# Performance work log

Hardware: AMD Instinct MI355X
Metric: run time of the kernel (lower is better)

## Reference

```python
import jax, jax.numpy as jnp
import numpy as np

K = 10
EPS = 1e-5
SLOPE = 0.01
B, FIN, FOUT, N = 16, 128, 128, 2048


def _bn(x, g, b, axes):
    # training-mode batchnorm over given axes (channel dim is axis 1)
    m = jnp.mean(x, axis=axes, keepdims=True)
    v = jnp.var(x, axis=axes, keepdims=True)
    sh = [1] * x.ndim
    sh[1] = -1
    return (x - m) * jax.lax.rsqrt(v + EPS) * g.reshape(sh) + b.reshape(sh)


def _lrelu(x):
    return jnp.where(x >= 0, x, SLOPE * x)


def _conv1x1(x, W, b):
    return jnp.einsum('bcnk,oc->bonk', x, W) + b[None, :, None, None]


def _forward(x, pc, Wf, bf, gf, betaf, Wx, bx, gx, betax, Wa1, ba1, ga1, beta_a1, Wa2, ba2, ga2, beta_a2, Wi, bi, gi, beta_i, W2, b2, g2, beta2):
    Bsz, Fin, Npts = x.shape
    k = K
    # --- kNN graph build: pairwise sq-dist via bmm, full sort, drop self ---
    sq = jnp.sum(x * x, axis=1)  # [B,N]
    dist = -2.0 * jnp.einsum('bdn,bdm->bnm', x, x) + sq[:, :, None] + sq[:, None, :]
    idx = jnp.argsort(dist, axis=2)[:, :, 1:k + 1]  # [B,N,k]
    gather = jax.vmap(lambda f, i: f[:, i])  # [C,N],[N,k] -> [C,N,k]
    nbr = gather(x, idx)
    nbr_xyz = gather(pc, idx)
    e_fea = jnp.concatenate([jnp.broadcast_to(x[..., None], (Bsz, Fin, Npts, k)), nbr - x[..., None]], axis=1)   # [B,2Fin,N,k]
    e_xyz = jnp.concatenate([jnp.broadcast_to(pc[..., None], (Bsz, 3, Npts, k)), nbr_xyz - pc[..., None]], axis=1)  # [B,6,N,k]
    # --- bilateral attention weights ---
    w = _lrelu(_bn(_conv1x1(e_fea, Wf, bf), gf, betaf, (0, 2, 3))) * _lrelu(_bn(_conv1x1(e_xyz, Wx, bx), gx, betax, (0, 2, 3)))
    w = _lrelu(_bn(_conv1x1(w, Wa1, ba1), ga1, beta_a1, (0, 2, 3)))
    w = _lrelu(_bn(_conv1x1(w, Wa2, ba2), ga2, beta_a2, (0, 2, 3)))
    w = jax.nn.softmax(w, axis=-1)  # [B,2Fin,N,k]
    # --- interpolation conv over neighbour axis (kernel [1, k//2+1]) ---
    inte = jax.lax.conv_general_dilated(e_fea, Wi, (1, 1), 'VALID', dimension_numbers=('NCHW', 'OIHW', 'NCHW')) + bi[None, :, None, None]
    inte = _lrelu(_bn(inte, gi, beta_i, (0, 2, 3)))  # [B,4Fin,N,k-k//2]
    inte = jnp.transpose(inte, (0, 2, 1, 3)).reshape(Bsz, Npts, 2 * Fin, k)  # channel-pair interleave, same layout as torch .view
    inte = jnp.transpose(inte, (0, 2, 1, 3)) * w  # [B,2Fin,N,k]
    merge = jnp.concatenate([e_fea, inte], axis=3)  # [B,2Fin,N,2k]
    # conv2: kernel [1,2k] spans full width -> width-1 output, as einsum
    out = jnp.einsum('bcnw,ocw->bon', merge, W2[:, :, 0, :]) + b2[None, :, None]  # [B,2Fout,N]
    out = jnp.maximum(_bn(out, g2, beta2, (0, 2)), 0.0)
    Fout = out.shape[1] // 2
    return out.reshape(Bsz, Fout, 2 * Npts)


def setup_inputs() -> dict:
    ks = jax.random.split(jax.random.key(0), 10)
    s = 0.05
    return {
        'x': jax.random.normal(ks[0], (B, FIN, N), jnp.float32),
        'pc': jax.random.normal(ks[1], (B, 3, N), jnp.float32),
        'Wf': jax.random.normal(ks[2], (16, 2 * FIN), jnp.float32) * s,
        'bf': jnp.zeros((16,), jnp.float32), 'gf': jnp.ones((16,), jnp.float32), 'betaf': jnp.zeros((16,), jnp.float32),
        'Wx': jax.random.normal(ks[3], (16, 6), jnp.float32) * s,
        'bx': jnp.zeros((16,), jnp.float32), 'gx': jnp.ones((16,), jnp.float32), 'betax': jnp.zeros((16,), jnp.float32),
        'Wa1': jax.random.normal(ks[4], (64, 16), jnp.float32) * s,
        'ba1': jnp.zeros((64,), jnp.float32), 'ga1': jnp.ones((64,), jnp.float32), 'beta_a1': jnp.zeros((64,), jnp.float32),
        'Wa2': jax.random.normal(ks[5], (2 * FIN, 64), jnp.float32) * s,
        'ba2': jnp.zeros((2 * FIN,), jnp.float32), 'ga2': jnp.ones((2 * FIN,), jnp.float32), 'beta_a2': jnp.zeros((2 * FIN,), jnp.float32),
        'Wi': jax.random.normal(ks[6], (4 * FIN, 2 * FIN, 1, K // 2 + 1), jnp.float32) * s,
        'bi': jnp.zeros((4 * FIN,), jnp.float32), 'gi': jnp.ones((4 * FIN,), jnp.float32), 'beta_i': jnp.zeros((4 * FIN,), jnp.float32),
        'W2': jax.random.normal(ks[7], (2 * FOUT, 2 * FIN, 1, 2 * K), jnp.float32) * s,
        'b2': jnp.zeros((2 * FOUT,), jnp.float32), 'g2': jnp.ones((2 * FOUT,), jnp.float32), 'beta2': jnp.zeros((2 * FOUT,), jnp.float32),
    }


def reference(x, pc, Wf, bf, gf, betaf, Wx, bx, gx, betax, Wa1, ba1, ga1, beta_a1, Wa2, ba2, ga2, beta_a2, Wi, bi, gi, beta_i, W2, b2, g2, beta2):
    return _forward(x, pc, Wf, bf, gf, betaf, Wx, bx, gx, betax, Wa1, ba1, ga1, beta_a1, Wa2, ba2, ga2, beta_a2, Wi, bi, gi, beta_i, W2, b2, g2, beta2)
```

## Files before the change

kernel.cpp:

```cpp
#include <hip/hip_runtime.h>
#include <hip/hip_bf16.h>
#include <cstdio>
#include <cstddef>

#define B_    16
#define FIN_  128
#define N_    2048
#define K_    10
#define EPS_  1e-5f
#define SLOPE_ 0.01f

typedef float f32x4 __attribute__((ext_vector_type(4)));
typedef short s16x8 __attribute__((ext_vector_type(8)));
typedef short s16x4 __attribute__((ext_vector_type(4)));

constexpr int SUM_F=0,   SS_F=16,   SUM_X=32,  SS_X=48;
constexpr int SUM_A1=64, SS_A1=128, SUM_A2=192,SS_A2=448;
constexpr int SUM_I=704, SS_I=1216, SUM_O=1728,SS_O=1984;
constexpr int SCALE_F=2240, SHIFT_F=2256, SCALE_X=2272, SHIFT_X=2288;
constexpr int SCALE_A1=2304, SHIFT_A1=2368, SCALE_A2=2432, SHIFT_A2=2688;
constexpr int SCALE_I=2944, SHIFT_I=3456, SCALE_O=3968, SHIFT_O=4224;
constexpr int STATS_TOTAL=4480;

constexpr int KW2_ = 3968;
constexpr int CHUNK_ = 8192;

__device__ __forceinline__ float lrelu(float v){ return v >= 0.f ? v : SLOPE_*v; }
__device__ __forceinline__ float wave_sum(float v){
  #pragma unroll
  for (int o = 32; o > 0; o >>= 1) v += __shfl_down(v, o, 64);
  return v;
}
__device__ __forceinline__ unsigned short f2bf(float f){
  __hip_bfloat16 h = __float2bfloat16(f);
  return *reinterpret_cast<unsigned short*>(&h);
}
__device__ __forceinline__ float bf2f(unsigned short u){
  __hip_bfloat16 h = *reinterpret_cast<__hip_bfloat16*>(&u);
  return __bfloat162float(h);
}

__global__ void k_zero(float* s){
  for (int i = threadIdx.x; i < STATS_TOTAL; i += 256) s[i] = 0.f;
}

__global__ __launch_bounds__(256) void k_xt(const float* __restrict__ x, float* __restrict__ xT){
  __shared__ float t[32][33];
  const int b = blockIdx.z;
  const int c0 = blockIdx.x*32, n0 = blockIdx.y*32;
  const int tx = threadIdx.x & 31, ty = threadIdx.x >> 5;
  #pragma unroll
  for (int s = 0; s < 32; s += 8)
    t[ty+s][tx] = x[((size_t)b*FIN_ + c0+ty+s)*N_ + n0 + tx];
  __syncthreads();
  #pragma unroll
  for (int s = 0; s < 32; s += 8)
    xT[((size_t)b*N_ + n0+ty+s)*FIN_ + c0 + tx] = t[tx][ty+s];
}

__global__ __launch_bounds__(256) void k_sq(const float* __restrict__ x, float* __restrict__ sq){
  int id = blockIdx.x*256 + threadIdx.x;
  int b = id >> 11, n = id & (N_-1);
  const float* xb = x + (size_t)b*FIN_*N_ + n;
  float part[16];
  #pragma unroll
  for (int p = 0; p < 16; ++p){
    float a = 0.f;
    #pragma unroll
    for (int q = 0; q < 8; ++q){
      float v = xb[(size_t)(p + 16*q)*N_];
      a = __fmaf_rn(v, v, a);
    }
    part[p] = a;
  }
  #pragma unroll
  for (int off = 8; off > 0; off >>= 1){
    #pragma unroll
    for (int l = 0; l < off; ++l)
      part[l] = __fadd_rn(part[l], part[l+off]);
  }
  sq[id] = part[0];
}

__global__ __launch_bounds__(256, 2) void k_knn(const float* __restrict__ x, const float* __restrict__ sq,
                                                int* __restrict__ idx){
  __shared__ __align__(16) char smem[61440];
  float* xi = (float*)smem;
  const int b = blockIdx.y, i0 = blockIdx.x*64;
  const float* xb = x + (size_t)b*FIN_*N_;
  for (int t = threadIdx.x; t < FIN_*64; t += 256){
    int c = t >> 6, ii = t & 63;
    xi[t] = xb[(size_t)c*N_ + i0 + ii];
  }
  __syncthreads();
  const int ty = threadIdx.x >> 4;
  const int tx = threadIdx.x & 15;
  const int ibase = ty*4;
  const f32x4 sqi = *(const f32x4*)&sq[b*N_ + i0 + ibase];
  float bd[4][10]; int bi[4][10];
  #pragma unroll
  for (int ii=0;ii<4;++ii)
    #pragma unroll
    for (int s=0;s<10;++s){ bd[ii][s] = 1e30f; bi[ii][s] = -1; }

  for (int j0 = 0; j0 < N_; j0 += 64){
    const int jb = j0 + tx*4;
    const float* xjp = xb + jb;
    f32x4 acc[4] = {};
    #pragma unroll 8
    for (int c = 0; c < FIN_; ++c){
      const f32x4 a  = *(const f32x4*)&xi[c*64 + ibase];
      const f32x4 bb = *(const f32x4*)&xjp[(size_t)c*N_];
      #pragma unroll
      for (int ii=0;ii<4;++ii){
        #pragma unroll
        for (int m=0;m<4;++m)
          acc[ii][m] = __fmaf_rn(a[ii], bb[m], acc[ii][m]);
      }
    }
    const f32x4 sqj = *(const f32x4*)&sq[b*N_ + jb];
    #pragma unroll
    for (int ii=0;ii<4;++ii){
      const int i = i0 + ibase + ii;
      #pragma unroll
      for (int m=0;m<4;++m){
        int j = jb + m;
        float d = __fadd_rn(__fadd_rn(__fmul_rn(-2.f, acc[ii][m]), sqi[ii]), sqj[m]);
        if (j == i) d = 1e30f;
        if (d < bd[ii][9]){
          bd[ii][9] = d; bi[ii][9] = j;
          #pragma unroll
          for (int s = 9; s > 0; --s){
            if (bd[ii][s] < bd[ii][s-1]){
              float td = bd[ii][s]; bd[ii][s] = bd[ii][s-1]; bd[ii][s-1] = td;
              int ti = bi[ii][s]; bi[ii][s] = bi[ii][s-1]; bi[ii][s-1] = ti;
            }
          }
        }
      }
    }
  }

  __syncthreads();
  float* dbuf = (float*)smem;
  unsigned short* ibuf = (unsigned short*)(smem + 40960);
  #pragma unroll
  for (int ii=0;ii<4;++ii)
    #pragma unroll
    for (int s=0;s<10;++s){
      dbuf[(tx*10+s)*64 + ibase+ii] = bd[ii][s];
      ibuf[(tx*10+s)*64 + ibase+ii] = (unsigned short)bi[ii][s];
    }
  __syncthreads();
  if (threadIdx.x < 64){
    const int rr = threadIdx.x;
    int p[16];
    #pragma unroll
    for (int qq=0;qq<16;++qq) p[qq]=0;
    int* op = idx + ((size_t)b*N_ + i0 + rr)*K_;
    for (int s = 0; s < K_; ++s){
      float dm = 1e38f; int im = 0x7fffffff; int qm = 0;
      #pragma unroll
      for (int qq = 0; qq < 16; ++qq){
        int pq = p[qq];
        float d  = (pq < 10) ? dbuf[(qq*10+pq)*64 + rr] : 1e38f;
        int   jd = (pq < 10) ? (int)ibuf[(qq*10+pq)*64 + rr] : 0x7fffffff;
        bool take = (d < dm) || (d == dm && jd < im);
        if (take){ dm = d; im = jd; qm = qq; }
      }
      #pragma unroll
      for (int qq = 0; qq < 16; ++qq) if (qm == qq) p[qq]++;
      op[s] = im;
    }
  }
}

__global__ __launch_bounds__(256) void k_fx_stats(const float* __restrict__ xT, const float* __restrict__ pc,
                                                  const int* __restrict__ idx,
                                                  const float* __restrict__ Wf, const float* __restrict__ Wx,
                                                  float* __restrict__ stats, float* __restrict__ ytmp){
  __shared__ float wfT[256*16];
  __shared__ float wxT[6*16];
  for (int t = threadIdx.x; t < 256*16; t += 256){ int c = t >> 4, o = t & 15; wfT[t] = Wf[o*256 + c]; }
  if (threadIdx.x < 96){ int cc = threadIdx.x >> 4, o = threadIdx.x & 15; wxT[cc*16+o] = Wx[o*6+cc]; }
  __syncthreads();
  const int id = blockIdx.x*256 + threadIdx.x;
  const int b = id >> 11, n = id & (N_-1);
  const float* xs = xT + (size_t)id*FIN_;
  const float* pb = pc + (size_t)b*3*N_;
  float yc[16];
  #pragma unroll
  for (int o=0;o<16;++o) yc[o]=0.f;
  for (int c=0;c<FIN_;c+=4){
    const f32x4 v4 = *(const f32x4*)&xs[c];
    #pragma unroll
    for (int e=0;e<4;++e){
      float v = v4[e];
      #pragma unroll
      for (int o=0;o<16;++o) yc[o] += wfT[(c+e)*16+o]*v;
    }
  }
  float p0=pb[n], p1=pb[N_+n], p2=pb[2*N_+n];
  float sf[16], ssf[16], sx[16], ssx[16];
  #pragma unroll
  for (int o=0;o<16;++o){ sf[o]=0.f;ssf[o]=0.f;sx[o]=0.f;ssx[o]=0.f; }
  for (int kk=0;kk<K_;++kk){
    int j = idx[(size_t)id*K_ + kk];
    const float* xj = xT + ((size_t)b*N_ + j)*FIN_;
    float y[16];
    #pragma unroll
    for (int o=0;o<16;++o) y[o]=yc[o];
    for (int c=0;c<FIN_;c+=4){
      const f32x4 a4 = *(const f32x4*)&xj[c];
      const f32x4 s4 = *(const f32x4*)&xs[c];
      #pragma unroll
      for (int e=0;e<4;++e){
        float d = a4[e]-s4[e];
        #pragma unroll
        for (int o=0;o<16;++o) y[o] += wfT[(128+c+e)*16+o]*d;
      }
    }
    float q0=pb[j]-p0, q1=pb[N_+j]-p1, q2=pb[2*N_+j]-p2;
    float vx[16];
    #pragma unroll
    for (int o=0;o<16;++o){
      vx[o] = wxT[0*16+o]*p0 + wxT[1*16+o]*p1 + wxT[2*16+o]*p2
            + wxT[3*16+o]*q0 + wxT[4*16+o]*q1 + wxT[5*16+o]*q2;
    }
    #pragma unroll
    for (int o=0;o<16;++o){
      sf[o]+=y[o]; ssf[o]+=y[o]*y[o];
      sx[o]+=vx[o]; ssx[o]+=vx[o]*vx[o];
    }
    float* yt = ytmp + ((size_t)id*K_ + kk)*32;
    #pragma unroll
    for (int o=0;o<16;++o){ yt[o] = y[o]; yt[16+o] = vx[o]; }
  }
  #pragma unroll
  for (int o=0;o<16;++o){
    float v;
    v = wave_sum(sf[o]);  if ((threadIdx.x&63)==0) atomicAdd(&stats[SUM_F+o], v);
    v = wave_sum(ssf[o]); if ((threadIdx.x&63)==0) atomicAdd(&stats[SS_F+o], v);
    v = wave_sum(sx[o]);  if ((threadIdx.x&63)==0) atomicAdd(&stats[SUM_X+o], v);
    v = wave_sum(ssx[o]); if ((threadIdx.x&63)==0) atomicAdd(&stats[SS_X+o], v);
  }
}

__global__ void k_finalize(float* stats, int sumoff, int ssoff, int nch, float cnt_inv,
                           const float* __restrict__ g, const float* __restrict__ bt,
                           int scoff, int shoff){
  int c = threadIdx.x;
  if (c < nch){
    float mean = stats[sumoff+c]*cnt_inv;
    float var  = stats[ssoff+c]*cnt_inv - mean*mean;
    float rstd = rsqrtf(var + EPS_);
    float sc = g[c]*rstd;
    stats[scoff+c] = sc;
    stats[shoff+c] = bt[c] - mean*sc;
  }
}

__global__ __launch_bounds__(256) void k_wapply(const float* __restrict__ ytmp, const float* __restrict__ stats,
                                                float* __restrict__ wprod){
  __shared__ float s4[64];
  if (threadIdx.x < 64) s4[threadIdx.x] = stats[SCALE_F + threadIdx.x];
  __syncthreads();
  const int e = blockIdx.x*256 + threadIdx.x;
  const float* yt = ytmp + (size_t)e*32;
  float* wp = wprod + (size_t)e*16;
  #pragma unroll
  for (int o=0;o<16;++o){
    float a  = lrelu(yt[o]*s4[o] + s4[16+o]);
    float bb = lrelu(yt[16+o]*s4[32+o] + s4[48+o]);
    wp[o] = a*bb;
  }
}

__global__ __launch_bounds__(256) void k_a1_stats(const float* __restrict__ wprod, const float* __restrict__ Wa1,
                                                  float* __restrict__ stats){
  __shared__ float wp[64*16];
  const int oc = threadIdx.x & 63, sub = threadIdx.x >> 6;
  float wa[16];
  #pragma unroll
  for (int j = 0; j < 16; ++j) wa[j] = Wa1[oc*16+j];
  float s = 0.f, ss = 0.f;
  for (int tile = blockIdx.x; tile < 5120; tile += gridDim.x){
    __syncthreads();
    for (int t = threadIdx.x; t < 1024; t += 256) wp[t] = wprod[(size_t)tile*1024 + t];
    __syncthreads();
    for (int p = sub*16; p < sub*16+16; ++p){
      float y = 0.f;
      #pragma unroll
      for (int j = 0; j < 16; ++j) y += wa[j]*wp[p*16+j];
      s += y; ss += y*y;
    }
  }
  atomicAdd(&stats[SUM_A1+oc], s);
  atomicAdd(&stats[SS_A1+oc], ss);
}

__global__ __launch_bounds__(256) void k_a2_stats(const float* __restrict__ wprod, const float* __restrict__ Wa1,
                                                  const float* __restrict__ Wa2, float* __restrict__ stats){
  __shared__ float wp[64*16];
  __shared__ float a1t[64*64];
  __shared__ float wa1T[16*64];
  __shared__ float sc1[64], sh1[64];
  for (int t=threadIdx.x;t<1024;t+=256){ int j=t&63, jj=t>>6; wa1T[jj*64+j] = Wa1[j*16+jj]; }
  if (threadIdx.x < 64){ sc1[threadIdx.x]=stats[SCALE_A1+threadIdx.x]; sh1[threadIdx.x]=stats[SHIFT_A1+threadIdx.x]; }
  const int oc = threadIdx.x;
  float wa2[64];
  #pragma unroll
  for (int j=0;j<64;++j) wa2[j] = Wa2[oc*64+j];
  float s=0.f, ss=0.f;
  for (int tile = blockIdx.x; tile < 5120; tile += gridDim.x){
    __syncthreads();
    for (int t=threadIdx.x;t<1024;t+=256) wp[t] = wprod[(size_t)tile*1024 + t];
    __syncthreads();
    for (int t=threadIdx.x;t<4096;t+=256){
      int p = t >> 6, j = t & 63;
      float yv=0.f;
      #pragma unroll
      for (int jj=0;jj<16;++jj) yv += wa1T[jj*64+j]*wp[p*16+jj];
      a1t[t] = lrelu(yv*sc1[j]+sh1[j]);
    }
    __syncthreads();
    #pragma unroll 4
    for (int p=0;p<64;++p){
      float yv=0.f;
      #pragma unroll
      for (int j=0;j<64;++j) yv += wa2[j]*a1t[p*64+j];
      s += yv; ss += yv*yv;
    }
  }
  atomicAdd(&stats[SUM_A2+oc], s);
  atomicAdd(&stats[SS_A2+oc], ss);
}

__global__ __launch_bounds__(256) void k_prepAi(const float* __restrict__ Wi, unsigned short* __restrict__ Ai){
  const int total = 512*896;
  for (int e = blockIdx.x*256 + threadIdx.x; e < total; e += gridDim.x*256){
    int o = e / 896, k = e - o*896;
    float v;
    if (k < 768){
      int u = k >> 7, c = k & 127;
      v = Wi[(size_t)o*1536 + (128+c)*6 + u];
    } else {
      const float* p = &Wi[(size_t)o*1536 + (size_t)(k-768)*6];
      v = p[0]+p[1]+p[2]+p[3]+p[4]+p[5];
    }
    Ai[e] = f2bf(v);
  }
}

__global__ __launch_bounds__(256) void k_prepA2(const float* __restrict__ W2,
                                                unsigned short* __restrict__ A2hi,
                                                unsigned short* __restrict__ A2lo){
  const int total = 256*KW2_;
  for (int e = blockIdx.x*256 + threadIdx.x; e < total; e += gridDim.x*256){
    int oc = e / KW2_, k = e - oc*KW2_;
    const float* wr = &W2[(size_t)oc*5120];
    float v;
    if (k < 2560){
      int o = k & 511, t5 = k >> 9;
      int cch = o >> 1, w = (o & 1)*5 + t5;
      v = wr[cch*20 + 10 + w];
    } else if (k < 3840){
      int kk = k - 2560; int w = kk >> 7, c = kk & 127;
      v = wr[(128+c)*20 + w];
    } else {
      int c = k - 3840;
      float s = 0.f;
      #pragma unroll
      for (int w = 0; w < 10; ++w) s += wr[c*20+w] - wr[(128+c)*20+w];
      v = s;
    }
    unsigned short hi = f2bf(v);
    float lo = v - bf2f(hi);
    A2hi[e] = hi;
    A2lo[e] = f2bf(lo);
  }
}

__global__ __launch_bounds__(256) void k_gather(const float* __restrict__ xT, const int* __restrict__ idx,
                                                unsigned short* __restrict__ Bd, int pxbase){
  const int e = blockIdx.x*256 + threadIdx.x;
  const int pxl = e >> 4, sub = e & 15;
  const int px = pxbase + pxl;
  const int c0 = sub*8;
  const float* xs = xT + (size_t)px*FIN_ + c0;
  const f32x4 s0 = *(const f32x4*)&xs[0];
  const f32x4 s1 = *(const f32x4*)&xs[4];
  unsigned short* bo = Bd + (size_t)pxl*1408;
  const size_t bb = (size_t)(px >> 11)*N_*FIN_;
  const int* ip = idx + (size_t)px*K_;
  #pragma unroll
  for (int w = 0; w < 10; ++w){
    int j = ip[w];
    const float* xj = xT + bb + (size_t)j*FIN_ + c0;
    const f32x4 a0 = *(const f32x4*)&xj[0];
    const f32x4 a1 = *(const f32x4*)&xj[4];
    unsigned short tw[8];
    tw[0]=f2bf(a0.x-s0.x); tw[1]=f2bf(a0.y-s0.y); tw[2]=f2bf(a0.z-s0.z); tw[3]=f2bf(a0.w-s0.w);
    tw[4]=f2bf(a1.x-s1.x); tw[5]=f2bf(a1.y-s1.y); tw[6]=f2bf(a1.z-s1.z); tw[7]=f2bf(a1.w-s1.w);
    *(s16x8*)&bo[w*128 + c0] = *(const s16x8*)tw;
  }
  unsigned short tw[8];
  tw[0]=f2bf(s0.x); tw[1]=f2bf(s0.y); tw[2]=f2bf(s0.z); tw[3]=f2bf(s0.w);
  tw[4]=f2bf(s1.x); tw[5]=f2bf(s1.y); tw[6]=f2bf(s1.z); tw[7]=f2bf(s1.w);
  *(s16x8*)&bo[1280 + c0] = *(const s16x8*)tw;
}

__global__ __launch_bounds__(256) void k_gemmI(const unsigned short* __restrict__ Bd,
                                               const unsigned short* __restrict__ Ai,
                                               __hip_bfloat16* __restrict__ ybuf, float* __restrict__ stats,
                                               int pxbase){
  __shared__ __align__(16) unsigned short As[128*72];
  __shared__ __align__(16) unsigned short Bs[128*72];
  const int o0 = blockIdx.x * 128;
  const int c0 = blockIdx.y * 128;
  const int t5 = blockIdx.z;
  const int rowA = threadIdx.x >> 1;
  const int kA   = (threadIdx.x & 1)*32;
  const unsigned short* arow = Ai + (size_t)(o0+rowA)*896 + kA;
  const int colJ = threadIdx.x >> 1;
  const int kB   = (threadIdx.x & 1)*32;
  const unsigned short* brow = Bd + (size_t)(c0 + colJ)*1408;
  const int wave = threadIdx.x >> 6, lane = threadIdx.x & 63;
  const int quad = lane >> 4, l16 = lane & 15;
  const int wm = wave & 1, wn = wave >> 1;

  f32x4 acc[4][4] = {};

  for (int k0 = 0; k0 < 896; k0 += 64){
    __syncthreads();
    {
      unsigned short* dst = &As[rowA*72 + kA];
      *(s16x8*)&dst[0]  = *(const s16x8*)&arow[k0+0];
      *(s16x8*)&dst[8]  = *(const s16x8*)&arow[k0+8];
      *(s16x8*)&dst[16] = *(const s16x8*)&arow[k0+16];
      *(s16x8*)&dst[24] = *(const s16x8*)&arow[k0+24];
    }
    {
      const int kk = k0 + kB;
      const unsigned short* src = brow + ((kk < 768) ? ((t5 + (kk >> 7))*128 + (kk & 127))
                                                     : (1280 + (kk - 768)));
      unsigned short* dst = &Bs[colJ*72 + kB];
      *(s16x8*)&dst[0]  = *(const s16x8*)&src[0];
      *(s16x8*)&dst[8]  = *(const s16x8*)&src[8];
      *(s16x8*)&dst[16] = *(const s16x8*)&src[16];
      *(s16x8*)&dst[24] = *(const s16x8*)&src[24];
    }
    __syncthreads();
    #pragma unroll
    for (int ks = 0; ks < 2; ++ks){
      s16x8 af[4], bfr[4];
      #pragma unroll
      for (int mt = 0; mt < 4; ++mt)
        af[mt] = *(const s16x8*)&As[(wm*64 + mt*16 + l16)*72 + ks*32 + quad*8];
      #pragma unroll
      for (int nt = 0; nt < 4; ++nt)
        bfr[nt] = *(const s16x8*)&Bs[(wn*64 + nt*16 + l16)*72 + ks*32 + quad*8];
      #pragma unroll
      for (int mt = 0; mt < 4; ++mt)
        #pragma unroll
        for (int nt = 0; nt < 4; ++nt)
          acc[mt][nt] = __builtin_amdgcn_mfma_f32_16x16x32_bf16(af[mt], bfr[nt], acc[mt][nt], 0, 0, 0);
    }
  }

  __syncthreads();
  float* red = (float*)As;
  red[threadIdx.x] = 0.f;
  __syncthreads();
  #pragma unroll
  for (int mt = 0; mt < 4; ++mt){
    const int rowLbase = wm*64 + mt*16 + quad*4;
    #pragma unroll
    for (int reg = 0; reg < 4; ++reg){
      float s = 0.f, ss = 0.f;
      #pragma unroll
      for (int nt = 0; nt < 4; ++nt){ float v = acc[mt][nt][reg]; s += v; ss += v*v; }
      atomicAdd(&red[(rowLbase+reg)*2+0], s);
      atomicAdd(&red[(rowLbase+reg)*2+1], ss);
    }
  }
  #pragma unroll
  for (int mt = 0; mt < 4; ++mt){
    #pragma unroll
    for (int nt = 0; nt < 4; ++nt){
      const int px = pxbase + c0 + wn*64 + nt*16 + l16;
      const int ob = wm*64 + mt*16 + quad*4;
      s16x4 w;
      #pragma unroll
      for (int reg = 0; reg < 4; ++reg) w[reg] = (short)f2bf(acc[mt][nt][reg]);
      *(s16x4*)&ybuf[(size_t)px*2560 + t5*512 + o0 + ob] = w;
    }
  }
  __syncthreads();
  if (threadIdx.x < 128){
    atomicAdd(&stats[SUM_I + o0 + threadIdx.x], red[threadIdx.x*2+0]);
    atomicAdd(&stats[SS_I + o0 + threadIdx.x], red[threadIdx.x*2+1]);
  }
}

__global__ __launch_bounds__(256, 4) void k_wchain(const float* __restrict__ wprod, const float* __restrict__ Wa1,
                                                   const float* __restrict__ Wa2, const float* __restrict__ stats,
                                                   __hip_bfloat16* __restrict__ ybuf, int pxPerBlk){
  __shared__ float wp[160];
  __shared__ float a1l[640];
  __shared__ float wa1T[16*64];
  __shared__ float sc1[64], sh1[64];
  for (int t = threadIdx.x; t < 1024; t += 256){ int j = t & 63, jj = t >> 6; wa1T[jj*64+j] = Wa1[j*16+jj]; }
  if (threadIdx.x < 64){ sc1[threadIdx.x]=stats[SCALE_A1+threadIdx.x]; sh1[threadIdx.x]=stats[SHIFT_A1+threadIdx.x]; }
  const int c = threadIdx.x;
  f32x4 wa2v[16];
  #pragma unroll
  for (int j4=0;j4<16;++j4) wa2v[j4] = *(const f32x4*)&Wa2[c*64 + j4*4];
  const float sc2 = stats[SCALE_A2+c], sh2 = stats[SHIFT_A2+c];
  const float sci0 = stats[SCALE_I + 2*c], shi0 = stats[SHIFT_I + 2*c];
  const float sci1 = stats[SCALE_I + 2*c+1], shi1 = stats[SHIFT_I + 2*c+1];

  for (int pp = 0; pp < pxPerBlk; ++pp){
    const size_t px = (size_t)blockIdx.x*pxPerBlk + pp;
    __syncthreads();
    if (threadIdx.x < 160) wp[threadIdx.x] = wprod[px*160 + threadIdx.x];
    __syncthreads();
    for (int t = threadIdx.x; t < 640; t += 256){
      int kk = t >> 6, j = t & 63;
      float y=0.f;
      #pragma unroll
      for (int jj=0;jj<16;++jj) y += wa1T[jj*64+j]*wp[kk*16+jj];
      a1l[kk*64+j] = lrelu(y*sc1[j]+sh1[j]);
    }
    __syncthreads();
    float wt[10];
    #pragma unroll
    for (int kk=0;kk<10;++kk){
      f32x4 acc = {0.f,0.f,0.f,0.f};
      #pragma unroll
      for (int j4=0;j4<16;++j4){
        const f32x4 a = *(const f32x4*)&a1l[kk*64 + j4*4];
        acc += wa2v[j4]*a;
      }
      float y = (acc.x+acc.y)+(acc.z+acc.w);
      wt[kk] = lrelu(y*sc2+sh2);
    }
    float mx = wt[0];
    #pragma unroll
    for (int kk=1;kk<10;++kk) mx = fmaxf(mx, wt[kk]);
    float sum = 0.f;
    #pragma unroll
    for (int kk=0;kk<10;++kk){ wt[kk] = __expf(wt[kk]-mx); sum += wt[kk]; }
    float inv = 1.f/sum;
    __hip_bfloat16* yb = ybuf + px*2560;
    #pragma unroll
    for (int q = 0; q < 10; ++q){
      const int t5q = (q < 5) ? q : q-5;
      const int ii  = t5q*512 + 2*c + ((q < 5) ? 0 : 1);
      float v = __bfloat162float(yb[ii]);
      float sc = (q < 5) ? sci0 : sci1;
      float sh = (q < 5) ? shi0 : shi1;
      yb[ii] = __float2bfloat16(lrelu(v*sc+sh) * (wt[q]*inv));
    }
  }
}

__global__ __launch_bounds__(256) void k_w2(const float* __restrict__ xT, const int* __restrict__ idx,
                                            const __hip_bfloat16* __restrict__ inte,
                                            const unsigned short* __restrict__ A2hi,
                                            const unsigned short* __restrict__ A2lo,
                                            float* __restrict__ outpre, float* __restrict__ stats){
  __shared__ __align__(16) unsigned short AsH[128*40];
  __shared__ __align__(16) unsigned short AsL[128*40];
  __shared__ __align__(16) unsigned short BsH[128*40];
  __shared__ __align__(16) unsigned short BsL[128*40];
  __shared__ int sIdx[128*10];
  const int r0 = blockIdx.x * 128;
  const int c0 = blockIdx.y * 128;
  for (int t = threadIdx.x; t < 1280; t += 256) sIdx[t] = idx[(size_t)c0*10 + t];
  const int rowA  = threadIdx.x >> 1;
  const int halfA = threadIdx.x & 1;
  const unsigned short* ahrow = A2hi + (size_t)(r0+rowA)*KW2_ + halfA*16;
  const unsigned short* alrow = A2lo + (size_t)(r0+rowA)*KW2_ + halfA*16;
  const int colJ  = threadIdx.x >> 1;
  const int cHalf = (threadIdx.x & 1)*16;
  const int pxJ   = c0 + colJ;
  const size_t selfJ  = (size_t)pxJ*FIN_;
  const size_t bbaseJ = (size_t)(pxJ >> 11)*N_*FIN_;
  const __hip_bfloat16* ibJ = inte + (size_t)pxJ*2560;
  const int wave = threadIdx.x >> 6, lane = threadIdx.x & 63;
  const int quad = lane >> 4, l16 = lane & 15;
  const int wm = wave & 1, wn = wave >> 1;

  f32x4 acc[4][4] = {};

  for (int k0 = 0; k0 < KW2_; k0 += 32){
    __syncthreads();
    {
      *(s16x8*)&AsH[rowA*40 + halfA*16]     = *(const s16x8*)&ahrow[k0];
      *(s16x8*)&AsH[rowA*40 + halfA*16 + 8] = *(const s16x8*)&ahrow[k0+8];
      *(s16x8*)&AsL[rowA*40 + halfA*16]     = *(const s16x8*)&alrow[k0];
      *(s16x8*)&AsL[rowA*40 + halfA*16 + 8] = *(const s16x8*)&alrow[k0+8];
    }
    if (k0 < 2560){
      *(s16x8*)&BsH[colJ*40 + cHalf]     = *(const s16x8*)(ibJ + k0 + cHalf);
      *(s16x8*)&BsH[colJ*40 + cHalf + 8] = *(const s16x8*)(ibJ + k0 + cHalf + 8);
    } else {
      const float* src;
      if (k0 < 3840){
        const int w  = (k0 - 2560) >> 7;
        const int cb = ((k0 - 2560) & 127) + cHalf;
        const int j  = sIdx[colJ*10 + w];
        src = &xT[bbaseJ + (size_t)j*FIN_ + cb];
      } else {
        src = &xT[selfJ + (k0 - 3840) + cHalf];
      }
      unsigned short th[16], tl[16];
      #pragma unroll
      for (int q = 0; q < 4; ++q){
        const f32x4 v = *(const f32x4*)&src[q*4];
        #pragma unroll
        for (int e2 = 0; e2 < 4; ++e2){
          float f = v[e2];
          unsigned short h = f2bf(f);
          float r = f - bf2f(h);
          th[q*4+e2] = h;
          tl[q*4+e2] = f2bf(r);
        }
      }
      *(s16x8*)&BsH[colJ*40 + cHalf]     = *(const s16x8*)&th[0];
      *(s16x8*)&BsH[colJ*40 + cHalf + 8] = *(const s16x8*)&th[8];
      *(s16x8*)&BsL[colJ*40 + cHalf]     = *(const s16x8*)&tl[0];
      *(s16x8*)&BsL[colJ*40 + cHalf + 8] = *(const s16x8*)&tl[8];
    }
    __syncthreads();
    s16x8 ah[4], al[4], bh[4];
    #pragma unroll
    for (int mt = 0; mt < 4; ++mt){
      ah[mt] = *(const s16x8*)&AsH[(wm*64 + mt*16 + l16)*40 + quad*8];
      al[mt] = *(const s16x8*)&AsL[(wm*64 + mt*16 + l16)*40 + quad*8];
    }
    #pragma unroll
    for (int nt = 0; nt < 4; ++nt)
      bh[nt] = *(const s16x8*)&BsH[(wn*64 + nt*16 + l16)*40 + quad*8];
    #pragma unroll
    for (int mt = 0; mt < 4; ++mt)
      #pragma unroll
      for (int nt = 0; nt < 4; ++nt){
        acc[mt][nt] = __builtin_amdgcn_mfma_f32_16x16x32_bf16(ah[mt], bh[nt], acc[mt][nt], 0, 0, 0);
        acc[mt][nt] = __builtin_amdgcn_mfma_f32_16x16x32_bf16(al[mt], bh[nt], acc[mt][nt], 0, 0, 0);
      }
    if (k0 >= 2560){
      s16x8 bl[4];
      #pragma unroll
      for (int nt = 0; nt < 4; ++nt)
        bl[nt] = *(const s16x8*)&BsL[(wn*64 + nt*16 + l16)*40 + quad*8];
      #pragma unroll
      for (int mt = 0; mt < 4; ++mt)
        #pragma unroll
        for (int nt = 0; nt < 4; ++nt)
          acc[mt][nt] = __builtin_amdgcn_mfma_f32_16x16x32_bf16(ah[mt], bl[nt], acc[mt][nt], 0, 0, 0);
    }
  }

  __syncthreads();
  float* red = (float*)AsH;
  red[threadIdx.x] = 0.f;
  __syncthreads();
  #pragma unroll
  for (int mt = 0; mt < 4; ++mt){
    const int rowLbase = wm*64 + mt*16 + quad*4;
    #pragma unroll
    for (int reg = 0; reg < 4; ++reg){
      float s = 0.f, ss = 0.f;
      #pragma unroll
      for (int nt = 0; nt < 4; ++nt){ float v = acc[mt][nt][reg]; s += v; ss += v*v; }
      atomicAdd(&red[(rowLbase+reg)*2+0], s);
      atomicAdd(&red[(rowLbase+reg)*2+1], ss);
    }
  }
  #pragma unroll
  for (int mt = 0; mt < 4; ++mt){
    #pragma unroll
    for (int nt = 0; nt < 4; ++nt){
      const int col = c0 + wn*64 + nt*16 + l16;
      const int rowb = r0 + wm*64 + mt*16 + quad*4;
      #pragma unroll
      for (int reg = 0; reg < 4; ++reg)
        outpre[(size_t)(rowb+reg)*32768 + col] = acc[mt][nt][reg];
    }
  }
  __syncthreads();
  if (threadIdx.x < 128){
    atomicAdd(&stats[SUM_O + r0 + threadIdx.x], red[threadIdx.x*2+0]);
    atomicAdd(&stats[SS_O + r0 + threadIdx.x], red[threadIdx.x*2+1]);
  }
}

__global__ __launch_bounds__(256) void k_final(const float* __restrict__ outpre, const float* __restrict__ stats,
                                               float* __restrict__ out){
  const unsigned total = (unsigned)B_*128u*4096u;
  for (unsigned e = blockIdx.x*256u + threadIdx.x; e < total; e += gridDim.x*256u){
    unsigned b = e >> 19;
    unsigned rem = e & ((1u<<19)-1u);
    unsigned f = rem >> 12;
    unsigned m = rem & 4095u;
    unsigned half = m >> 11;
    unsigned n = m & 2047u;
    unsigned c = f*2u + half;
    float pre = outpre[(size_t)c*32768 + b*2048 + n];
    float v = pre*stats[SCALE_O+c] + stats[SHIFT_O+c];
    out[e] = fmaxf(v, 0.f);
  }
}

extern "C" void kernel_launch(void* const* d_in, const int* in_sizes, int n_in,
                              void* d_out, int out_size, void* d_ws, size_t ws_size,
                              hipStream_t stream) {
  (void)in_sizes; (void)n_in; (void)out_size;
  const float* x    = (const float*)d_in[0];
  const float* pc   = (const float*)d_in[1];
  const float* Wf   = (const float*)d_in[2];
  const float* gf   = (const float*)d_in[4];
  const float* btf  = (const float*)d_in[5];
  const float* Wx   = (const float*)d_in[6];
  const float* gx   = (const float*)d_in[8];
  const float* btx  = (const float*)d_in[9];
  const float* Wa1  = (const float*)d_in[10];
  const float* ga1  = (const float*)d_in[12];
  const float* bta1 = (const float*)d_in[13];
  const float* Wa2  = (const float*)d_in[14];
  const float* ga2  = (const float*)d_in[16];
  const float* bta2 = (const float*)d_in[17];
  const float* Wi   = (const float*)d_in[18];
  const float* gi   = (const float*)d_in[20];
  const float* bti  = (const float*)d_in[21];
  const float* W2   = (const float*)d_in[22];
  const float* g2   = (const float*)d_in[24];
  const float* bt2  = (const float*)d_in[25];
  float* out = (float*)d_out;

  char* ws = (char*)d_ws;
  float*  stats  = (float*)ws;
  int*    idx    = (int*)  (ws + 32768);
  float*  sq     = (float*)(ws + 1343488);
  float*  wprod  = (float*)(ws + 1605632);
  float*  xT     = (float*)(ws + 22577152);
  unsigned short* A2hi = (unsigned short*)(ws + 39354368);
  unsigned short* A2lo = (unsigned short*)(ws + 41385984);
  float*  outpre = (float*)(ws + 44597248);
  unsigned short* Ai = (unsigned short*)(ws + 44597248);
  unsigned short* Bd = (unsigned short*)(ws + 45645824);
  __hip_bfloat16* ybuf = (__hip_bfloat16*)(ws + 78151680);
  float* ytmp = (float*)(ws + 78151680);
  if (ws_size < 245923840ULL) {
    fprintf(stderr, "kernel_launch: ws_size %zu < required 245923840\n", ws_size);
    return;
  }

  k_zero<<<1, 256, 0, stream>>>(stats);
  k_xt<<<dim3(FIN_/32, N_/32, B_), 256, 0, stream>>>(x, xT);
  k_sq<<<(B_*N_)/256, 256, 0, stream>>>(x, sq);
  k_knn<<<dim3(N_/64, B_), 256, 0, stream>>>(x, sq, idx);
  k_prepAi<<<1024, 256, 0, stream>>>(Wi, Ai);
  k_prepA2<<<1024, 256, 0, stream>>>(W2, A2hi, A2lo);

  k_fx_stats<<<(B_*N_)/256, 256, 0, stream>>>(xT, pc, idx, Wf, Wx, stats, ytmp);
  k_finalize<<<1, 512, 0, stream>>>(stats, SUM_F, SS_F, 16, 1.f/327680.f, gf, btf, SCALE_F, SHIFT_F);
  k_finalize<<<1, 512, 0, stream>>>(stats, SUM_X, SS_X, 16, 1.f/327680.f, gx, btx, SCALE_X, SHIFT_X);

  k_wapply<<<1280, 256, 0, stream>>>(ytmp, stats, wprod);
  k_a1_stats<<<512, 256, 0, stream>>>(wprod, Wa1, stats);
  k_finalize<<<1, 512, 0, stream>>>(stats, SUM_A1, SS_A1, 64, 1.f/327680.f, ga1, bta1, SCALE_A1, SHIFT_A1);

  k_a2_stats<<<512, 256, 0, stream>>>(wprod, Wa1, Wa2, stats);
  k_finalize<<<1, 512, 0, stream>>>(stats, SUM_A2, SS_A2, 256, 1.f/327680.f, ga2, bta2, SCALE_A2, SHIFT_A2);

  for (int ch = 0; ch < (B_*N_)/CHUNK_; ++ch){
    k_gather<<<(CHUNK_*16)/256, 256, 0, stream>>>(xT, idx, Bd, ch*CHUNK_);
    k_gemmI<<<dim3(4, CHUNK_/128, 5), 256, 0, stream>>>(Bd, Ai, ybuf, stats, ch*CHUNK_);
  }
  k_finalize<<<1, 512, 0, stream>>>(stats, SUM_I, SS_I, 512, 1.f/163840.f, gi, bti, SCALE_I, SHIFT_I);

  k_wchain<<<2048, 256, 0, stream>>>(wprod, Wa1, Wa2, stats, ybuf, (B_*N_)/2048);

  k_w2<<<dim3(2, 256), 256, 0, stream>>>(xT, idx, ybuf, A2hi, A2lo, outpre, stats);
  k_finalize<<<1, 512, 0, stream>>>(stats, SUM_O, SS_O, 256, 1.f/32768.f, g2, bt2, SCALE_O, SHIFT_O);

  k_final<<<4096, 256, 0, stream>>>(outpre, stats, out);
}
```

Before: 2.346 ms.

## Compute a2 BN stats via Gram matrix and split fx_stats neighbors across threads

```diff
diff --git a/kernel.cpp b/kernel.cpp
--- a/kernel.cpp
+++ b/kernel.cpp
@@ -21,6 +21,7 @@
 constexpr int SCALE_A1=2304, SHIFT_A1=2368, SCALE_A2=2432, SHIFT_A2=2688;
 constexpr int SCALE_I=2944, SHIFT_I=3456, SCALE_O=3968, SHIFT_O=4224;
 constexpr int STATS_TOTAL=4480;
+constexpr int AUX_TOTAL = 64 + 4096;
 
 constexpr int KW2_ = 3968;
 constexpr int CHUNK_ = 8192;
@@ -40,8 +41,9 @@
   return __bfloat162float(h);
 }
 
-__global__ void k_zero(float* s){
+__global__ void k_zero(float* s, float* aux){
   for (int i = threadIdx.x; i < STATS_TOTAL; i += 256) s[i] = 0.f;
+  for (int i = threadIdx.x; i < AUX_TOTAL; i += 256) aux[i] = 0.f;
 }
 
 __global__ __launch_bounds__(256) void k_xt(const float* __restrict__ x, float* __restrict__ xT){
@@ -184,7 +186,8 @@
   for (int t = threadIdx.x; t < 256*16; t += 256){ int c = t >> 4, o = t & 15; wfT[t] = Wf[o*256 + c]; }
   if (threadIdx.x < 96){ int cc = threadIdx.x >> 4, o = threadIdx.x & 15; wxT[cc*16+o] = Wx[o*6+cc]; }
   __syncthreads();
-  const int id = blockIdx.x*256 + threadIdx.x;
+  const int half = threadIdx.x >> 6;
+  const int id = blockIdx.x*64 + (threadIdx.x & 63);
   const int b = id >> 11, n = id & (N_-1);
   const float* xs = xT + (size_t)id*FIN_;
   const float* pb = pc + (size_t)b*3*N_;
@@ -204,7 +207,7 @@
   float sf[16], ssf[16], sx[16], ssx[16];
   #pragma unroll
   for (int o=0;o<16;++o){ sf[o]=0.f;ssf[o]=0.f;sx[o]=0.f;ssx[o]=0.f; }
-  for (int kk=0;kk<K_;++kk){
+  for (int kk=half; kk<K_; kk+=4){
     int j = idx[(size_t)id*K_ + kk];
     const float* xj = xT + ((size_t)b*N_ + j)*FIN_;
     float y[16];
@@ -299,19 +302,18 @@
   atomicAdd(&stats[SS_A1+oc], ss);
 }
 
-__global__ __launch_bounds__(256) void k_a2_stats(const float* __restrict__ wprod, const float* __restrict__ Wa1,
-                                                  const float* __restrict__ Wa2, float* __restrict__ stats){
+__global__ __launch_bounds__(256) void k_a2g(const float* __restrict__ wprod, const float* __restrict__ Wa1,
+                                             const float* __restrict__ stats, float* __restrict__ aux){
   __shared__ float wp[64*16];
   __shared__ float a1t[64*64];
   __shared__ float wa1T[16*64];
   __shared__ float sc1[64], sh1[64];
   for (int t=threadIdx.x;t<1024;t+=256){ int j=t&63, jj=t>>6; wa1T[jj*64+j] = Wa1[j*16+jj]; }
   if (threadIdx.x < 64){ sc1[threadIdx.x]=stats[SCALE_A1+threadIdx.x]; sh1[threadIdx.x]=stats[SHIFT_A1+threadIdx.x]; }
-  const int oc = threadIdx.x;
-  float wa2[64];
-  #pragma unroll
-  for (int j=0;j<64;++j) wa2[j] = Wa2[oc*64+j];
-  float s=0.f, ss=0.f;
+  const int i  = threadIdx.x >> 2;
+  const int jq = threadIdx.x & 3;
+  f32x4 g0={0.f,0.f,0.f,0.f}, g1={0.f,0.f,0.f,0.f}, g2={0.f,0.f,0.f,0.f}, g3={0.f,0.f,0.f,0.f};
+  float s = 0.f;
   for (int tile = blockIdx.x; tile < 5120; tile += gridDim.x){
     __syncthreads();
     for (int t=threadIdx.x;t<1024;t+=256) wp[t] = wprod[(size_t)tile*1024 + t];
@@ -326,14 +328,48 @@
     __syncthreads();
     #pragma unroll 4
     for (int p=0;p<64;++p){
-      float yv=0.f;
-      #pragma unroll
-      for (int j=0;j<64;++j) yv += wa2[j]*a1t[p*64+j];
-      s += yv; ss += yv*yv;
-    }
-  }
-  atomicAdd(&stats[SUM_A2+oc], s);
-  atomicAdd(&stats[SS_A2+oc], ss);
+      const float ai = a1t[p*64 + i];
+      const f32x4* row = (const f32x4*)&a1t[p*64 + jq*16];
+      g0 += ai*row[0]; g1 += ai*row[1]; g2 += ai*row[2]; g3 += ai*row[3];
+      if (jq == 0) s += ai;
+    }
+  }
+  float* G = aux + 64;
+  const int base = i*64 + jq*16;
+  #pragma unroll
+  for (int r=0;r<4;++r){ atomicAdd(&G[base+r],    g0[r]); }
+  #pragma unroll
+  for (int r=0;r<4;++r){ atomicAdd(&G[base+4+r],  g1[r]); }
+  #pragma unroll
+  for (int r=0;r<4;++r){ atomicAdd(&G[base+8+r],  g2[r]); }
+  #pragma unroll
+  for (int r=0;r<4;++r){ atomicAdd(&G[base+12+r], g3[r]); }
+  if (jq == 0) atomicAdd(&aux[i], s);
+}
+
+__global__ void k_a2fin(const float* __restrict__ aux, const float* __restrict__ Wa2,
+                        float* __restrict__ stats){
+  __shared__ float G[4096];
+  __shared__ float S[64];
+  for (int t = threadIdx.x; t < 4096; t += 256) G[t] = aux[64 + t];
+  if (threadIdx.x < 64) S[threadIdx.x] = aux[threadIdx.x];
+  __syncthreads();
+  const int oc = threadIdx.x;
+  float w[64];
+  #pragma unroll
+  for (int j=0;j<64;++j) w[j] = Wa2[oc*64+j];
+  float sum = 0.f;
+  #pragma unroll
+  for (int j=0;j<64;++j) sum += w[j]*S[j];
+  float ss = 0.f;
+  for (int i=0;i<64;++i){
+    float gi = 0.f;
+    #pragma unroll
+    for (int j=0;j<64;++j) gi += w[j]*G[i*64+j];
+    ss += w[i]*gi;
+  }
+  stats[SUM_A2+oc] = sum;
+  stats[SS_A2+oc]  = ss;
 }
 
 __global__ __launch_bounds__(256) void k_prepAi(const float* __restrict__ Wi, unsigned short* __restrict__ Ai){
@@ -744,6 +780,7 @@
   float*  stats  = (float*)ws;
   int*    idx    = (int*)  (ws + 32768);
   float*  sq     = (float*)(ws + 1343488);
+  float*  aux    = (float*)(ws + 1474560);
   float*  wprod  = (float*)(ws + 1605632);
   float*  xT     = (float*)(ws + 22577152);
   unsigned short* A2hi = (unsigned short*)(ws + 39354368);
@@ -758,14 +795,14 @@
     return;
   }
 
-  k_zero<<<1, 256, 0, stream>>>(stats);
+  k_zero<<<1, 256, 0, stream>>>(stats, aux);
   k_xt<<<dim3(FIN_/32, N_/32, B_), 256, 0, stream>>>(x, xT);
   k_sq<<<(B_*N_)/256, 256, 0, stream>>>(x, sq);
   k_knn<<<dim3(N_/64, B_), 256, 0, stream>>>(x, sq, idx);
   k_prepAi<<<1024, 256, 0, stream>>>(Wi, Ai);
   k_prepA2<<<1024, 256, 0, stream>>>(W2, A2hi, A2lo);
 
-  k_fx_stats<<<(B_*N_)/256, 256, 0, stream>>>(xT, pc, idx, Wf, Wx, stats, ytmp);
+  k_fx_stats<<<(B_*N_)/64, 256, 0, stream>>>(xT, pc, idx, Wf, Wx, stats, ytmp);
   k_finalize<<<1, 512, 0, stream>>>(stats, SUM_F, SS_F, 16, 1.f/327680.f, gf, btf, SCALE_F, SHIFT_F);
   k_finalize<<<1, 512, 0, stream>>>(stats, SUM_X, SS_X, 16, 1.f/327680.f, gx, btx, SCALE_X, SHIFT_X);
 
@@ -773,7 +810,8 @@
   k_a1_stats<<<512, 256, 0, stream>>>(wprod, Wa1, stats);
   k_finalize<<<1, 512, 0, stream>>>(stats, SUM_A1, SS_A1, 64, 1.f/327680.f, ga1, bta1, SCALE_A1, SHIFT_A1);
 
-  k_a2_stats<<<512, 256, 0, stream>>>(wprod, Wa1, Wa2, stats);
+  k_a2g<<<512, 256, 0, stream>>>(wprod, Wa1, stats, aux);
+  k_a2fin<<<1, 256, 0, stream>>>(aux, Wa2, stats);
   k_finalize<<<1, 512, 0, stream>>>(stats, SUM_A2, SS_A2, 256, 1.f/327680.f, ga2, bta2, SCALE_A2, SHIFT_A2);
 
   for (int ch = 0; ch < (B_*N_)/CHUNK_; ++ch){
```

Result: slower. 2.829 ms (+20.6%).
